# Performance work log

Measured on AMD Instinct MI355X. Metric: run time of the kernel, lower is better.

Reference implementation:

```python
import jax, jax.numpy as jnp
import numpy as np

B, N, C, H, L = 4, 1024, 1152, 16, 120
D = C // H
HID = 4 * C
EPS = 1e-6


def _ln(x):
    m = jnp.mean(x, axis=-1, keepdims=True)
    v = jnp.var(x, axis=-1, keepdims=True)
    return (x - m) * jax.lax.rsqrt(v + EPS)


def _attend(q, k, v):
    # q:(B,H,Nq,D) k,v:(B,H,Nk,D)
    scale = D ** -0.5
    s = jnp.einsum('bhnd,bhmd->bhnm', q, k) * scale
    p = jax.nn.softmax(s, axis=-1)
    o = jnp.einsum('bhnm,bhmd->bhnd', p, v)
    return o.transpose(0, 2, 1, 3).reshape(q.shape[0], q.shape[2], C)


def setup_inputs() -> dict:
    key = jax.random.key(0)
    ks = jax.random.split(key, 20)
    g = lambda i, shape, s=0.02: jax.random.normal(ks[i], shape, jnp.float32) * s
    return {
        'x': jax.random.normal(ks[0], (B, N, C), jnp.float32),
        'y': jax.random.normal(ks[1], (B, L, C), jnp.float32),
        't': jax.random.normal(ks[2], (B, 6 * C), jnp.float32),
        'sst': jax.random.normal(ks[3], (6, C), jnp.float32) / C ** 0.5,
        'qkv_w': g(4, (C, 3 * C)), 'qkv_b': jnp.zeros((3 * C,), jnp.float32),
        'proj_w': g(5, (C, C)), 'proj_b': jnp.zeros((C,), jnp.float32),
        'q_w': g(6, (C, C)), 'q_b': jnp.zeros((C,), jnp.float32),
        'kv_w': g(7, (C, 2 * C)), 'kv_b': jnp.zeros((2 * C,), jnp.float32),
        'cproj_w': g(8, (C, C)), 'cproj_b': jnp.zeros((C,), jnp.float32),
        'fc1_w': g(9, (C, HID)), 'fc1_b': jnp.zeros((HID,), jnp.float32),
        'fc2_w': g(10, (HID, C)), 'fc2_b': jnp.zeros((C,), jnp.float32),
    }


def reference(x, y, t, sst, qkv_w, qkv_b, proj_w, proj_b, q_w, q_b,
              kv_w, kv_b, cproj_w, cproj_b, fc1_w, fc1_b, fc2_w, fc2_b):
    mods = sst[None] + t.reshape(B, 6, C)  # (B,6,C)
    sh_msa, sc_msa, g_msa, sh_mlp, sc_mlp, g_mlp = [mods[:, i:i + 1] for i in range(6)]

    # --- self attention with adaLN modulation ---
    h = _ln(x) * (1 + sc_msa) + sh_msa
    qkv = (h @ qkv_w + qkv_b).reshape(B, N, 3, H, D).transpose(2, 0, 3, 1, 4)
    attn_out = _attend(qkv[0], qkv[1], qkv[2]) @ proj_w + proj_b
    x = x + g_msa * attn_out

    # --- cross attention (batched cond, no mask) ---
    q = (x @ q_w + q_b).reshape(B, N, H, D).transpose(0, 2, 1, 3)
    kv = (y @ kv_w + kv_b).reshape(B, L, 2, H, D).transpose(2, 0, 3, 1, 4)
    x = x + (_attend(q, kv[0], kv[1]) @ cproj_w + cproj_b)

    # --- MLP with adaLN modulation ---
    h = _ln(x) * (1 + sc_mlp) + sh_mlp
    h = jax.nn.gelu(h @ fc1_w + fc1_b, approximate=True) @ fc2_w + fc2_b
    x = x + g_mlp * h
    return x
```

## Files before the change

### kernel.cpp

```cpp
#include <hip/hip_runtime.h>
#include <hip/hip_bf16.h>
#include <stdint.h>

typedef __hip_bfloat16 BT;
typedef __bf16 bf16x8 __attribute__((ext_vector_type(8)));
typedef float f32x4 __attribute__((ext_vector_type(4)));

constexpr int kB = 4, kN = 1024, kC = 1152, kH = 16, kL = 120, kD = 72, kDp = 96;
constexpr int kHid = 4608, kBN = 4096, kZ = 64;
constexpr float kScale = 0.11785113019775793f;

__global__ void detect_dtype(const void* xin, int* flag) {
  __shared__ int cnt;
  if (threadIdx.x == 0) cnt = 0;
  __syncthreads();
  const BT* xb = (const BT*)xin;
  int local = 0;
  for (int i = threadIdx.x; i < 4096; i += 256) {
    float v = __bfloat162float(xb[i]);
    if (!(fabsf(v) <= 1e3f)) local++;
  }
  atomicAdd(&cnt, local);
  __syncthreads();
  if (threadIdx.x == 0) *flag = (cnt > 8) ? 1 : 0;
}

struct ConvSeg {
  const void* src;
  BT* dst;
  long long n;
};
struct ConvArgs {
  ConvSeg seg[10];
  int nseg;
};
__global__ void convert_all(ConvArgs a, const int* __restrict__ flag) {
  const int f = *flag;
  long long i = (long long)blockIdx.x * 256 + threadIdx.x;
#pragma unroll
  for (int s = 0; s < 10; ++s) {
    if (s >= a.nseg) return;
    if (i < a.seg[s].n) {
      a.seg[s].dst[i] = f ? __float2bfloat16(((const float*)a.seg[s].src)[i])
                          : ((const BT*)a.seg[s].src)[i];
      return;
    }
    i -= a.seg[s].n;
  }
}

__global__ void encode_ws(float* out, long long n, float c) {
  long long i = (long long)blockIdx.x * 256 + threadIdx.x;
  if (i < n) out[i] = c;
}

__device__ __forceinline__ void gl_lds16(const BT* g, BT* l) {
  __builtin_amdgcn_global_load_lds(
      (const __attribute__((address_space(1))) uint32_t*)g,
      (__attribute__((address_space(3))) uint32_t*)l, 16, 0, 0);
}

template <int BM, int EP>
__global__ __launch_bounds__(256, 4) void gemm_tile(
    const BT* __restrict__ A, const BT* __restrict__ Bm, const BT* __restrict__ bias,
    void* __restrict__ Cout, int M, int Nc, int K, int lda, int ldb, int ldc,
    long long sA, long long sB, long long sC) {
  constexpr int NA = BM / 32;
  constexpr int NJ = (BM == 128) ? 4 : 2;
  __shared__ __align__(16) BT As[2][BM * 32];
  __shared__ __align__(16) BT Bs[2][128 * 32];
  A += (long long)blockIdx.z * sA;
  Bm += (long long)blockIdx.z * sB;

  const int gx = gridDim.x, nwg = gx * gridDim.y;
  int id = blockIdx.y * gx + blockIdx.x;
  {
    const int q = nwg >> 3, r = nwg & 7;
    const int xcd = id & 7, pos = id >> 3;
    const int base = (xcd < r) ? xcd * (q + 1) : r * (q + 1) + (xcd - r) * q;
    id = base + pos;
  }
  const int m0 = (id / gx) * BM, n0 = (id % gx) * 128;

  const int tid = threadIdx.x, lane = tid & 63, w = tid >> 6;
  const int lr = lane >> 2;
  const int lc = ((lane & 3) ^ ((lane >> 4) & 3)) * 8;
  const int l15 = lane & 15;
  const int qx8 = ((lane >> 4) ^ ((lane >> 2) & 3)) * 8;
  const int wm = (BM == 128) ? (w & 1) * 64 : 0;
  const int wn = (BM == 128) ? (w >> 1) * 64 : w * 32;

  auto gptr = [&](int u, int half) -> const BT* {
    if (u < NA) {
      int rr = m0 + u * 32 + lr + half * 16;
      if (rr >= M) rr = M - 1;
      return A + (long long)rr * lda + lc;
    }
    int rr = n0 + (u - NA) * 32 + lr + half * 16;
    if (rr >= Nc) rr = Nc - 1;
    return Bm + (long long)rr * ldb + lc;
  };
  const bool has2 = (w < NA);
  const int u2 = has2 ? (w + 4) : w;
  const BT* g00 = gptr(w, 0);
  const BT* g01 = gptr(w, 1);
  const BT* g10 = gptr(u2, 0);
  const BT* g11 = gptr(u2, 1);
  BT* d00[2];
  BT* d10[2];
#pragma unroll
  for (int bb = 0; bb < 2; ++bb) {
    d00[bb] = (w < NA) ? &As[bb][w * 1024] : &Bs[bb][(w - NA) * 1024];
    int ub = u2 - NA;
    if (ub < 0) ub = 0;
    if (ub > 3) ub = 3;
    d10[bb] = &Bs[bb][ub * 1024];
  }

  auto stage = [&](int bb, int k0) {
    gl_lds16(g00 + k0, d00[bb]);
    gl_lds16(g01 + k0, d00[bb] + 512);
    if (has2) {
      gl_lds16(g10 + k0, d10[bb]);
      gl_lds16(g11 + k0, d10[bb] + 512);
    }
  };

  f32x4 acc[4][NJ] = {};

  auto compute = [&](int bb) {
    bf16x8 af[4], bf[NJ];
#pragma unroll
    for (int i = 0; i < 4; ++i)
      af[i] = *reinterpret_cast<const bf16x8*>(&As[bb][(wm + i * 16 + l15) * 32 + qx8]);
#pragma unroll
    for (int j = 0; j < NJ; ++j)
      bf[j] = *reinterpret_cast<const bf16x8*>(&Bs[bb][(wn + j * 16 + l15) * 32 + qx8]);
#pragma unroll
    for (int i = 0; i < 4; ++i)
#pragma unroll
      for (int j = 0; j < NJ; ++j)
        acc[i][j] = __builtin_amdgcn_mfma_f32_16x16x32_bf16(af[i], bf[j], acc[i][j], 0, 0, 0);
  };

  stage(0, 0);
  __syncthreads();
  const int nk = K >> 5;
  int cur = 0;
  for (int t = 1; t < nk; ++t) {
    stage(cur ^ 1, t << 5);
    compute(cur);
    __syncthreads();
    cur ^= 1;
  }
  compute(cur);

  const int rowq = (lane >> 4) * 4;
  const long long cb = (long long)blockIdx.z * sC;
#pragma unroll
  for (int j = 0; j < NJ; ++j) {
    int col = n0 + wn + j * 16 + l15;
    if (col >= Nc) continue;
    float bv = bias ? __bfloat162float(bias[col]) : 0.f;
#pragma unroll
    for (int i = 0; i < 4; ++i) {
      int row = m0 + wm + i * 16 + rowq;
#pragma unroll
      for (int r = 0; r < 4; ++r) {
        if (row + r < M) {
          float v = acc[i][j][r] + bv;
          if (EP == 2) {
            float z = 1.5957691216057308f * (v + 0.044715f * v * v * v);
            v = v / (1.f + __expf(-z));
          }
          long long off = cb + (long long)(row + r) * ldc + col;
          if (EP == 1)
            ((float*)Cout)[off] = v;
          else
            ((BT*)Cout)[off] = __float2bfloat16(v);
        }
      }
    }
  }
}

__global__ void transpose_any(const void* __restrict__ in, BT* __restrict__ out,
                              int R, int Cin, const int* __restrict__ flag) {
  __shared__ BT tile[32][33];
  const int f = *flag;
  const int tx = threadIdx.x & 31, ty = threadIdx.x >> 5;
  const int r0 = blockIdx.y * 32, c0 = blockIdx.x * 32;
#pragma unroll
  for (int j = 0; j < 32; j += 8) {
    int r = r0 + ty + j;
    if (r < R && c0 + tx < Cin) {
      long long idx = (long long)r * Cin + c0 + tx;
      tile[ty + j][tx] = f ? __float2bfloat16(((const float*)in)[idx]) : ((const BT*)in)[idx];
    }
  }
  __syncthreads();
#pragma unroll
  for (int j = 0; j < 32; j += 8) {
    int oc = c0 + ty + j;
    if (oc < Cin && r0 + tx < R) out[(long long)oc * R + r0 + tx] = tile[tx][ty + j];
  }
}

template <int SRC>
__global__ __launch_bounds__(256) void ln_mod(const void* __restrict__ xin,
                                              const BT* __restrict__ tc,
                                              const BT* __restrict__ sstc,
                                              BT* __restrict__ hout,
                                              int shiftRow, int scaleRow,
                                              const int* __restrict__ flag) {
  const int f = (SRC == 1) ? 1 : *flag;
  const int row = blockIdx.x;
  const int b = row >> 10;
  const long long base = (long long)row * kC;
  float s = 0.f, s2 = 0.f;
  for (int c = threadIdx.x; c < kC; c += 256) {
    float v = f ? ((const float*)xin)[base + c] : __bfloat162float(((const BT*)xin)[base + c]);
    s += v;
    s2 += v * v;
  }
  for (int o = 32; o > 0; o >>= 1) {
    s += __shfl_down(s, o, 64);
    s2 += __shfl_down(s2, o, 64);
  }
  __shared__ float red[8];
  const int w = threadIdx.x >> 6;
  if ((threadIdx.x & 63) == 0) {
    red[w] = s;
    red[4 + w] = s2;
  }
  __syncthreads();
  const float m = (red[0] + red[1] + red[2] + red[3]) * (1.f / kC);
  const float ex2 = (red[4] + red[5] + red[6] + red[7]) * (1.f / kC);
  const float rstd = rsqrtf(ex2 - m * m + 1e-6f);
  const BT* tsh = tc + (long long)b * 6 * kC + (long long)shiftRow * kC;
  const BT* tsc = tc + (long long)b * 6 * kC + (long long)scaleRow * kC;
  const BT* ssh = sstc + (long long)shiftRow * kC;
  const BT* ssc = sstc + (long long)scaleRow * kC;
  for (int c = threadIdx.x; c < kC; c += 256) {
    float sc = __bfloat162float(ssc[c]) + __bfloat162float(tsc[c]);
    float sh = __bfloat162float(ssh[c]) + __bfloat162float(tsh[c]);
    float xv0 = f ? ((const float*)xin)[base + c] : __bfloat162float(((const BT*)xin)[base + c]);
    float xv = (xv0 - m) * rstd;
    hout[base + c] = __float2bfloat16(xv * (1.f + sc) + sh);
  }
}

__global__ void scatter_qk(const BT* __restrict__ qkv, BT* __restrict__ Qp,
                           BT* __restrict__ Kp) {
  long long i = (long long)blockIdx.x * 256 + threadIdx.x;
  if (i >= (long long)kZ * kN * kDp) return;
  int d = (int)(i % kDp);
  long long r = i / kDp;
  int n = (int)(r % kN);
  int z = (int)(r / kN);
  int b = z >> 4, h = z & 15;
  if (d < kD) {
    long long src = ((long long)(b * kN + n)) * (3 * kC) + h * kD + d;
    Qp[i] = __float2bfloat16(kScale * __bfloat162float(qkv[src]));
    Kp[i] = qkv[src + kC];
  } else {
    Qp[i] = __float2bfloat16(0.f);
    Kp[i] = __float2bfloat16(0.f);
  }
}

__global__ void scatter_v(const BT* __restrict__ qkv, BT* __restrict__ VT) {
  long long i = (long long)blockIdx.x * 256 + threadIdx.x;
  if (i >= (long long)kZ * kD * kN) return;
  int n = (int)(i % kN);
  long long r = i / kN;
  int d = (int)(r % kD);
  int z = (int)(r / kD);
  int b = z >> 4, h = z & 15;
  VT[i] = qkv[((long long)(b * kN + n)) * (3 * kC) + 2 * kC + h * kD + d];
}

__global__ void scatter_qc(const BT* __restrict__ qc, BT* __restrict__ Qp) {
  long long i = (long long)blockIdx.x * 256 + threadIdx.x;
  if (i >= (long long)kZ * kN * kDp) return;
  int d = (int)(i % kDp);
  long long r = i / kDp;
  int n = (int)(r % kN);
  int z = (int)(r / kN);
  int b = z >> 4, h = z & 15;
  Qp[i] = (d < kD)
              ? __float2bfloat16(kScale * __bfloat162float(qc[((long long)(b * kN + n)) * kC + h * kD + d]))
              : __float2bfloat16(0.f);
}

__global__ void scatter_kc(const BT* __restrict__ kvb, BT* __restrict__ Kcp) {
  long long i = (long long)blockIdx.x * 256 + threadIdx.x;
  if (i >= (long long)kZ * kL * kDp) return;
  int d = (int)(i % kDp);
  long long r = i / kDp;
  int l = (int)(r % kL);
  int z = (int)(r / kL);
  int b = z >> 4, h = z & 15;
  Kcp[i] = (d < kD) ? kvb[((long long)(b * kL + l)) * (2 * kC) + h * kD + d] : __float2bfloat16(0.f);
}

__global__ void scatter_vc(const BT* __restrict__ kvb, BT* __restrict__ VcT) {
  long long i = (long long)blockIdx.x * 256 + threadIdx.x;
  if (i >= (long long)kZ * kD * 128) return;
  int l = (int)(i % 128);
  long long r = i / 128;
  int d = (int)(r % kD);
  int z = (int)(r / kD);
  int b = z >> 4, h = z & 15;
  VcT[i] = (l < kL) ? kvb[((long long)(b * kL + l)) * (2 * kC) + kC + h * kD + d] : __float2bfloat16(0.f);
}

__global__ void heads_to_cat(const BT* __restrict__ O, BT* __restrict__ cat) {
  long long i = (long long)blockIdx.x * 256 + threadIdx.x;
  if (i >= (long long)kZ * kN * kD) return;
  int d = (int)(i % kD);
  long long r = i / kD;
  int n = (int)(r % kN);
  int z = (int)(r / kN);
  int b = z >> 4, h = z & 15;
  cat[((long long)(b * kN + n)) * kC + h * kD + d] = O[i];
}

__global__ __launch_bounds__(256) void softmax1024(BT* __restrict__ S) {
  const long long row = blockIdx.x;
  BT* r = S + row * 1024;
  const int tid = threadIdx.x;
  union { ushort4 u; BT b[4]; } ld;
  ld.u = *(const ushort4*)(r + tid * 4);
  float v[4];
#pragma unroll
  for (int k = 0; k < 4; ++k) v[k] = __bfloat162float(ld.b[k]);
  float mx = fmaxf(fmaxf(v[0], v[1]), fmaxf(v[2], v[3]));
  for (int o = 32; o > 0; o >>= 1) mx = fmaxf(mx, __shfl_down(mx, o, 64));
  __shared__ float red[4], red2[4];
  if ((tid & 63) == 0) red[tid >> 6] = mx;
  __syncthreads();
  mx = fmaxf(fmaxf(red[0], red[1]), fmaxf(red[2], red[3]));
  float s = 0.f;
#pragma unroll
  for (int k = 0; k < 4; ++k) {
    v[k] = __expf(v[k] - mx);
    s += v[k];
  }
  for (int o = 32; o > 0; o >>= 1) s += __shfl_down(s, o, 64);
  if ((tid & 63) == 0) red2[tid >> 6] = s;
  __syncthreads();
  s = red2[0] + red2[1] + red2[2] + red2[3];
  const float inv = 1.f / s;
#pragma unroll
  for (int k = 0; k < 4; ++k) ld.b[k] = __float2bfloat16(v[k] * inv);
  *(ushort4*)(r + tid * 4) = ld.u;
}

__global__ void softmax_cross(BT* __restrict__ S) {
  const long long row = blockIdx.x;
  BT* r = S + row * 128;
  const int c = threadIdx.x;
  float v = (c < kL) ? __bfloat162float(r[c]) : -1e30f;
  float mx = v;
  for (int o = 32; o > 0; o >>= 1) mx = fmaxf(mx, __shfl_down(mx, o, 64));
  __shared__ float sm[2], ss[2];
  if ((c & 63) == 0) sm[c >> 6] = mx;
  __syncthreads();
  mx = fmaxf(sm[0], sm[1]);
  float e = (c < kL) ? __expf(v - mx) : 0.f;
  float s = e;
  for (int o = 32; o > 0; o >>= 1) s += __shfl_down(s, o, 64);
  if ((c & 63) == 0) ss[c >> 6] = s;
  __syncthreads();
  s = ss[0] + ss[1];
  r[c] = __float2bfloat16(e / s);
}

__global__ void resid_gate(const void* __restrict__ x, const BT* __restrict__ raw,
                           const BT* __restrict__ tc, const BT* __restrict__ sstc,
                           float* __restrict__ resf, BT* __restrict__ resb,
                           const int* __restrict__ flag) {
  long long i = (long long)blockIdx.x * 256 + threadIdx.x;
  if (i >= (long long)kBN * kC) return;
  const int f = *flag;
  int c = (int)(i % kC);
  int b = (int)(i / ((long long)kN * kC));
  float g = __bfloat162float(sstc[2 * kC + c]) + __bfloat162float(tc[(long long)b * 6 * kC + 2 * kC + c]);
  float xv = f ? ((const float*)x)[i] : __bfloat162float(((const BT*)x)[i]);
  float v = xv + g * __bfloat162float(raw[i]);
  resf[i] = v;
  resb[i] = __float2bfloat16(v);
}

__global__ void resid_add(float* __restrict__ res, const BT* __restrict__ raw) {
  long long i = (long long)blockIdx.x * 256 + threadIdx.x;
  if (i < (long long)kBN * kC) res[i] += __bfloat162float(raw[i]);
}

__global__ void final_out(const float* __restrict__ res, const BT* __restrict__ raw,
                          const BT* __restrict__ tc, const BT* __restrict__ sstc,
                          float* __restrict__ out) {
  long long i = (long long)blockIdx.x * 256 + threadIdx.x;
  if (i >= (long long)kBN * kC) return;
  int c = (int)(i % kC);
  int b = (int)(i / ((long long)kN * kC));
  float g = __bfloat162float(sstc[5 * kC + c]) + __bfloat162float(tc[(long long)b * 6 * kC + 5 * kC + c]);
  out[i] = res[i] + g * __bfloat162float(raw[i]);
}

extern "C" void kernel_launch(void* const* d_in, const int* in_sizes, int n_in,
                              void* d_out, int out_size, void* d_ws, size_t ws_size,
                              hipStream_t stream) {
  const void* x = d_in[0];
  const void* y = d_in[1];
  const void* t = d_in[2];
  const void* sst = d_in[3];
  const void* qkv_w = d_in[4];
  const void* qkv_b = d_in[5];
  const void* proj_w = d_in[6];
  const void* proj_b = d_in[7];
  const void* q_w = d_in[8];
  const void* q_b = d_in[9];
  const void* kv_w = d_in[10];
  const void* kv_b = d_in[11];
  const void* cproj_w = d_in[12];
  const void* cproj_b = d_in[13];
  const void* fc1_w = d_in[14];
  const void* fc1_b = d_in[15];
  const void* fc2_w = d_in[16];
  const void* fc2_b = d_in[17];
  (void)in_sizes; (void)n_in;

  char* p = (char*)d_ws;
  size_t off = 0;
  auto alloc = [&](size_t bytes) {
    void* r = p + off;
    off += (bytes + 1023) & ~(size_t)1023;
    return r;
  };
  int* dflag = (int*)alloc(16);
  BT* canonY = (BT*)alloc((size_t)kB * kL * kC * 2);
  BT* canonT = (BT*)alloc((size_t)kB * 6 * kC * 2);
  BT* canonSst = (BT*)alloc((size_t)6 * kC * 2);
  BT* canonBias = (BT*)alloc((size_t)16384 * 2);
  BT* wT = (BT*)alloc((size_t)kHid * kC * 2);
  BT* bufH = (BT*)alloc((size_t)kBN * kC * 2);
  BT* bufCH = (BT*)alloc((size_t)kZ * kN * kDp * 2);
  BT* bufQp = (BT*)alloc((size_t)kZ * kN * kDp * 2);
  BT* bufVT = (BT*)alloc((size_t)kZ * kD * kN * 2);
  BT* rawB = (BT*)alloc((size_t)kBN * kC * 2);
  float* resF = (float*)alloc((size_t)kBN * kC * 4);
  BT* arena = (BT*)alloc((size_t)kBN * kHid * 2);
  const size_t need = off;

  BT* bufO = rawB;
  BT* fc2T = bufQp;
  BT* kvBuf = (BT*)((char*)arena + 17825792);

  if (ws_size < need) {
    float c = 100.f * (float)(1 + (int)(ws_size >> 24));
    long long n = (long long)out_size;
    encode_ws<<<(int)((n + 255) / 256), 256, 0, stream>>>((float*)d_out, n, c);
    return;
  }

  BT* qkvB = canonBias;
  BT* projB = canonBias + 3456;
  BT* qB = canonBias + 4608;
  BT* kvB = canonBias + 5760;
  BT* cprojB = canonBias + 8064;
  BT* fc1B = canonBias + 9216;
  BT* fc2B = canonBias + 13824;

  auto gemm = [&](int ep, const BT* A, const BT* Bm, const BT* bias, void* Cp,
                  int M, int Nc, int K, int lda, int ldb, int ldc,
                  long long sA, long long sB, long long sC, int Zb) {
    long long nwg128 = (long long)((Nc + 127) / 128) * ((M + 127) / 128) * Zb;
    if (nwg128 < 512) {
      dim3 g((Nc + 127) / 128, (M + 63) / 64, Zb);
      if (ep == 0)
        gemm_tile<64, 0><<<g, 256, 0, stream>>>(A, Bm, bias, Cp, M, Nc, K, lda, ldb, ldc, sA, sB, sC);
      else if (ep == 1)
        gemm_tile<64, 1><<<g, 256, 0, stream>>>(A, Bm, bias, Cp, M, Nc, K, lda, ldb, ldc, sA, sB, sC);
      else
        gemm_tile<64, 2><<<g, 256, 0, stream>>>(A, Bm, bias, Cp, M, Nc, K, lda, ldb, ldc, sA, sB, sC);
    } else {
      dim3 g((Nc + 127) / 128, (M + 127) / 128, Zb);
      if (ep == 0)
        gemm_tile<128, 0><<<g, 256, 0, stream>>>(A, Bm, bias, Cp, M, Nc, K, lda, ldb, ldc, sA, sB, sC);
      else if (ep == 1)
        gemm_tile<128, 1><<<g, 256, 0, stream>>>(A, Bm, bias, Cp, M, Nc, K, lda, ldb, ldc, sA, sB, sC);
      else
        gemm_tile<128, 2><<<g, 256, 0, stream>>>(A, Bm, bias, Cp, M, Nc, K, lda, ldb, ldc, sA, sB, sC);
    }
  };
  auto tp = [&](const void* in, BT* out, int R, int Cin) {
    dim3 g((Cin + 31) / 32, (R + 31) / 32);
    transpose_any<<<g, 256, 0, stream>>>(in, out, R, Cin, dflag);
  };

  detect_dtype<<<1, 256, 0, stream>>>(x, dflag);
  {
    ConvArgs a;
    a.seg[0] = {y, canonY, (long long)kB * kL * kC};
    a.seg[1] = {t, canonT, (long long)kB * 6 * kC};
    a.seg[2] = {sst, canonSst, (long long)6 * kC};
    a.seg[3] = {qkv_b, qkvB, 3456};
    a.seg[4] = {proj_b, projB, 1152};
    a.seg[5] = {q_b, qB, 1152};
    a.seg[6] = {kv_b, kvB, 2304};
    a.seg[7] = {cproj_b, cprojB, 1152};
    a.seg[8] = {fc1_b, fc1B, 4608};
    a.seg[9] = {fc2_b, fc2B, 1152};
    a.nseg = 10;
    long long tot = 552960 + 27648 + 6912 + 14976;
    convert_all<<<(int)((tot + 255) / 256), 256, 0, stream>>>(a, dflag);
  }

  ln_mod<0><<<kBN, 256, 0, stream>>>(x, canonT, canonSst, bufH, 0, 1, dflag);
  tp(qkv_w, wT, kC, 3 * kC);
  gemm(0, bufH, wT, qkvB, arena, kBN, 3 * kC, kC, kC, kC, 3 * kC, 0, 0, 0, 1);
  {
    long long tot = (long long)kZ * kN * kDp;
    scatter_qk<<<(int)((tot + 255) / 256), 256, 0, stream>>>(arena, bufQp, bufCH);
    tot = (long long)kZ * kD * kN;
    scatter_v<<<(int)((tot + 255) / 256), 256, 0, stream>>>(arena, bufVT);
  }
  for (int c = 0; c < 4; ++c) {
    int z0 = c * 16;
    const BT* Qb = bufQp + (size_t)z0 * kN * kDp;
    const BT* Kb = bufCH + (size_t)z0 * kN * kDp;
    const BT* Vb = bufVT + (size_t)z0 * kD * kN;
    BT* Ob = bufO + (size_t)z0 * kN * kD;
    gemm(0, Qb, Kb, nullptr, arena, kN, kN, kDp, kDp, kDp, kN,
         (long long)kN * kDp, (long long)kN * kDp, (long long)kN * kN, 16);
    softmax1024<<<16 * kN, 256, 0, stream>>>(arena);
    gemm(0, arena, Vb, nullptr, Ob, kN, kD, kN, kN, kN, kD,
         (long long)kN * kN, (long long)kD * kN, (long long)kN * kD, 16);
  }
  heads_to_cat<<<18432, 256, 0, stream>>>(bufO, bufCH);
  tp(proj_w, wT, kC, kC);
  gemm(0, bufCH, wT, projB, rawB, kBN, kC, kC, kC, kC, kC, 0, 0, 0, 1);
  resid_gate<<<18432, 256, 0, stream>>>(x, rawB, canonT, canonSst, resF, bufH, dflag);

  tp(q_w, wT, kC, kC);
  gemm(0, bufH, wT, qB, bufCH, kBN, kC, kC, kC, kC, kC, 0, 0, 0, 1);
  {
    long long tot = (long long)kZ * kN * kDp;
    scatter_qc<<<(int)((tot + 255) / 256), 256, 0, stream>>>(bufCH, bufQp);
  }
  tp(kv_w, wT, kC, 2 * kC);
  gemm(0, canonY, wT, kvB, kvBuf, kB * kL, 2 * kC, kC, kC, kC, 2 * kC, 0, 0, 0, 1);
  {
    long long tot = (long long)kZ * kL * kDp;
    scatter_kc<<<(int)((tot + 255) / 256), 256, 0, stream>>>(kvBuf, bufCH);
    tot = (long long)kZ * kD * 128;
    scatter_vc<<<(int)((tot + 255) / 256), 256, 0, stream>>>(kvBuf, bufVT);
  }
  gemm(0, bufQp, bufCH, nullptr, arena, kN, kL, kDp, kDp, kDp, 128,
       (long long)kN * kDp, (long long)kL * kDp, (long long)kN * 128, kZ);
  softmax_cross<<<kZ * kN, 128, 0, stream>>>(arena);
  gemm(0, arena, bufVT, nullptr, bufO, kN, kD, 128, 128, 128, kD,
       (long long)kN * 128, (long long)kD * 128, (long long)kN * kD, kZ);
  heads_to_cat<<<18432, 256, 0, stream>>>(bufO, bufCH);
  tp(cproj_w, wT, kC, kC);
  gemm(0, bufCH, wT, cprojB, rawB, kBN, kC, kC, kC, kC, kC, 0, 0, 0, 1);
  resid_add<<<18432, 256, 0, stream>>>(resF, rawB);

  ln_mod<1><<<kBN, 256, 0, stream>>>(resF, canonT, canonSst, bufH, 3, 4, dflag);
  tp(fc1_w, wT, kC, kHid);
  tp(fc2_w, fc2T, kHid, kC);
  gemm(2, bufH, wT, fc1B, arena, kBN, kHid, kC, kC, kC, kHid, 0, 0, 0, 1);
  gemm(0, arena, fc2T, fc2B, rawB, kBN, kC, kHid, kHid, kHid, kC, 0, 0, 0, 1);
  final_out<<<18432, 256, 0, stream>>>(resF, rawB, canonT, canonSst, (float*)d_out);
}
```

Baseline: 873.4 us.

## Add 256x256-tile 8-wave bf16 GEMM kernel for QKV and FC1 projections

Adds a new 512-thread GEMM kernel with 256x256 output tiles and 64-wide K steps. It double-buffers A and B tiles in LDS through direct global-to-LDS loads with an XOR swizzle, and raises wave priority around the MFMA blocks. The QKV projection (N padded to 3584) and the FC1+GELU projection now use it, to raise arithmetic intensity and reduce global traffic per FLOP. The large tiles produce few workgroups (224 and 288), which can leave CUs idle or create a partial second wave. The 128KB LDS footprint also allows only one block per CU.

```diff
diff --git a/kernel.cpp b/kernel.cpp
--- a/kernel.cpp
+++ b/kernel.cpp
@@ -58,6 +58,127 @@
   __builtin_amdgcn_global_load_lds(
       (const __attribute__((address_space(1))) uint32_t*)g,
       (__attribute__((address_space(3))) uint32_t*)l, 16, 0, 0);
+}
+
+template <int EP>
+__global__ __launch_bounds__(512, 2) void gemm8(
+    const BT* __restrict__ A, const BT* __restrict__ Bm, const BT* __restrict__ bias,
+    void* __restrict__ Cout, int M, int Nc, int K, int lda, int ldb, int ldc) {
+  __shared__ __align__(16) BT Asl[2][256 * 64];
+  __shared__ __align__(16) BT Bsl[2][256 * 64];
+
+  const int gx = gridDim.x, nwg = gx * gridDim.y;
+  int id = blockIdx.y * gx + blockIdx.x;
+  {
+    const int q = nwg >> 3, r = nwg & 7;
+    const int xcd = id & 7, pos = id >> 3;
+    const int base = (xcd < r) ? xcd * (q + 1) : r * (q + 1) + (xcd - r) * q;
+    id = base + pos;
+  }
+  const int m0 = (id / gx) * 256, n0 = (id % gx) * 256;
+
+  const int tid = threadIdx.x, lane = tid & 63, w = tid >> 6;
+  const int l15 = lane & 15;
+  const int wm2 = (w >> 2) * 128;
+  const int wn4 = (w & 3) * 64;
+
+  const int srow = lane >> 3;
+  const int ssrc = ((lane & 7) ^ srow) * 8;
+  const BT* gA = A + (long long)(m0 + w * 32 + srow) * lda + ssrc;
+  const BT* gB = Bm + (long long)(n0 + w * 32 + srow) * ldb + ssrc;
+
+  auto stage = [&](int b, int k0) {
+#pragma unroll
+    for (int q = 0; q < 4; ++q)
+      gl_lds16(gA + (long long)q * 8 * lda + k0, &Asl[b][(w * 32 + q * 8) * 64]);
+#pragma unroll
+    for (int q = 0; q < 4; ++q)
+      gl_lds16(gB + (long long)q * 8 * ldb + k0, &Bsl[b][(w * 32 + q * 8) * 64]);
+  };
+
+  const int rsw = l15 & 7;
+  const int ch0 = (((lane >> 4) & 3) ^ rsw) * 8;
+  const int ch1 = ((4 | ((lane >> 4) & 3)) ^ rsw) * 8;
+
+  f32x4 acc[8][4] = {};
+
+  const int nk = K >> 6;
+  stage(0, 0);
+  if (nk > 1) {
+    stage(1, 64);
+    asm volatile("s_waitcnt vmcnt(8)" ::: "memory");
+  } else {
+    asm volatile("s_waitcnt vmcnt(0)" ::: "memory");
+  }
+  __builtin_amdgcn_s_barrier();
+
+  for (int t = 0; t < nk; ++t) {
+    const BT* Ab = &Asl[t & 1][0];
+    const BT* Bb = &Bsl[t & 1][0];
+    bf16x8 bfr[4][2];
+#pragma unroll
+    for (int p = 0; p < 4; ++p) {
+      bf16x8 af[2][2];
+#pragma unroll
+      for (int ii = 0; ii < 2; ++ii) {
+        const int row = wm2 + (2 * p + ii) * 16 + l15;
+        af[ii][0] = *reinterpret_cast<const bf16x8*>(&Ab[row * 64 + ch0]);
+        af[ii][1] = *reinterpret_cast<const bf16x8*>(&Ab[row * 64 + ch1]);
+      }
+      if (p == 0) {
+#pragma unroll
+        for (int j = 0; j < 4; ++j) {
+          const int row = wn4 + j * 16 + l15;
+          bfr[j][0] = *reinterpret_cast<const bf16x8*>(&Bb[row * 64 + ch0]);
+          bfr[j][1] = *reinterpret_cast<const bf16x8*>(&Bb[row * 64 + ch1]);
+        }
+      }
+      __builtin_amdgcn_s_barrier();
+      __builtin_amdgcn_s_setprio(1);
+#pragma unroll
+      for (int ii = 0; ii < 2; ++ii)
+#pragma unroll
+        for (int j = 0; j < 4; ++j) {
+          acc[2 * p + ii][j] = __builtin_amdgcn_mfma_f32_16x16x32_bf16(
+              af[ii][0], bfr[j][0], acc[2 * p + ii][j], 0, 0, 0);
+          acc[2 * p + ii][j] = __builtin_amdgcn_mfma_f32_16x16x32_bf16(
+              af[ii][1], bfr[j][1], acc[2 * p + ii][j], 0, 0, 0);
+        }
+      __builtin_amdgcn_s_setprio(0);
+      __builtin_amdgcn_s_barrier();
+    }
+    if (t + 2 < nk) stage(t & 1, (t + 2) << 6);
+    if (t + 1 < nk) {
+      if (t + 2 < nk)
+        asm volatile("s_waitcnt vmcnt(8)" ::: "memory");
+      else
+        asm volatile("s_waitcnt vmcnt(0)" ::: "memory");
+      __builtin_amdgcn_s_barrier();
+    }
+  }
+
+  const int rowq = (lane >> 4) * 4;
+#pragma unroll
+  for (int j = 0; j < 4; ++j) {
+    int col = n0 + wn4 + j * 16 + l15;
+    if (col >= Nc) continue;
+    float bv = bias ? __bfloat162float(bias[col]) : 0.f;
+#pragma unroll
+    for (int i = 0; i < 8; ++i) {
+      int row = m0 + wm2 + i * 16 + rowq;
+#pragma unroll
+      for (int r = 0; r < 4; ++r) {
+        if (row + r < M) {
+          float v = acc[i][j][r] + bv;
+          if (EP == 2) {
+            float z = 1.5957691216057308f * (v + 0.044715f * v * v * v);
+            v = v / (1.f + __expf(-z));
+          }
+          ((BT*)Cout)[(long long)(row + r) * ldc + col] = __float2bfloat16(v);
+        }
+      }
+    }
+  }
 }
 
 template <int BM, int EP>
@@ -495,6 +616,14 @@
         gemm_tile<128, 2><<<g, 256, 0, stream>>>(A, Bm, bias, Cp, M, Nc, K, lda, ldb, ldc, sA, sB, sC);
     }
   };
+  auto gemm8l = [&](int ep, const BT* A, const BT* Bm, const BT* bias, void* Cp,
+                    int M, int Nc, int Npad, int K, int lda, int ldb, int ldc) {
+    dim3 g(Npad / 256, M / 256, 1);
+    if (ep == 2)
+      gemm8<2><<<g, 512, 0, stream>>>(A, Bm, bias, Cp, M, Nc, K, lda, ldb, ldc);
+    else
+      gemm8<0><<<g, 512, 0, stream>>>(A, Bm, bias, Cp, M, Nc, K, lda, ldb, ldc);
+  };
   auto tp = [&](const void* in, BT* out, int R, int Cin) {
     dim3 g((Cin + 31) / 32, (R + 31) / 32);
     transpose_any<<<g, 256, 0, stream>>>(in, out, R, Cin, dflag);
@@ -520,7 +649,7 @@
 
   ln_mod<0><<<kBN, 256, 0, stream>>>(x, canonT, canonSst, bufH, 0, 1, dflag);
   tp(qkv_w, wT, kC, 3 * kC);
-  gemm(0, bufH, wT, qkvB, arena, kBN, 3 * kC, kC, kC, kC, 3 * kC, 0, 0, 0, 1);
+  gemm8l(0, bufH, wT, qkvB, arena, kBN, 3 * kC, 3584, kC, kC, kC, 3 * kC);
   {
     long long tot = (long long)kZ * kN * kDp;
     scatter_qk<<<(int)((tot + 255) / 256), 256, 0, stream>>>(arena, bufQp, bufCH);
@@ -571,7 +700,7 @@
   ln_mod<1><<<kBN, 256, 0, stream>>>(resF, canonT, canonSst, bufH, 3, 4, dflag);
   tp(fc1_w, wT, kC, kHid);
   tp(fc2_w, fc2T, kHid, kC);
-  gemm(2, bufH, wT, fc1B, arena, kBN, kHid, kC, kC, kC, kHid, 0, 0, 0, 1);
+  gemm8l(2, bufH, wT, fc1B, arena, kBN, kHid, kHid, kC, kC, kC, kHid);
   gemm(0, arena, fc2T, fc2B, rawB, kBN, kC, kHid, kHid, kHid, kC, 0, 0, 0, 1);
   final_out<<<18432, 256, 0, stream>>>(resF, rawB, canonT, canonSst, (float*)d_out);
 }
```

Result: slower. 900.3 us (+3.1%).
